# Kernel tuning notes

Hardware: AMD Instinct MI355X
Metric: run time of the kernel (lower is better)

Reference implementation:

```python
import jax, jax.numpy as jnp
import numpy as np

N_NODES = 100000
N_EDGES = 3200000
OUT_DIM = 128


def setup_inputs() -> dict:
    key = jax.random.key(0)
    k1, k2, k3, k4, k5, k6 = jax.random.split(key, 6)
    return {
        "previous_inclusion_score": jax.random.normal(k1, (N_NODES,), dtype=jnp.float32),
        "nodes": jax.random.normal(k2, (N_NODES, 3), dtype=jnp.float32),
        "row_indices": jax.random.randint(k3, (N_EDGES,), 0, N_NODES, dtype=jnp.int32),
        "col_indices": jax.random.randint(k4, (N_EDGES,), 0, N_NODES, dtype=jnp.int32),
        "W_phi": jax.random.normal(k5, (OUT_DIM,), dtype=jnp.float32),
        "W_theta": jax.random.normal(k6, (3, 1), dtype=jnp.float32),
    }


def reference(previous_inclusion_score, nodes, row_indices, col_indices, W_phi, W_theta):
    # gather endpoints and project 3D differences through W_theta: [E,3] @ [3,1] -> [E,1]
    diff = nodes[row_indices] - nodes[col_indices]
    proj = diff @ W_theta
    # torch.norm over dim=1 of an [E,1] tensor == abs
    neigh_distances = jnp.abs(proj[:, 0])  # [E]
    # per-node max over incident edges; empty segments -> -inf, original leaves them 0
    max_distances = jax.ops.segment_max(neigh_distances, row_indices, num_segments=N_NODES)
    max_distances = jnp.maximum(max_distances, 0.0)  # distances are >= 0, so this matches the zeros default
    # outer product with W_phi: [N, D]
    list_inc_score = W_phi[None, :] * max_distances[:, None]
    # previous_inclusion_score is non-empty and D != 1 -> mean over feature dim, then average with previous
    inc_mean = jnp.mean(list_inc_score, axis=1)  # [N]
    return 0.5 * (previous_inclusion_score + inc_mean)
```

## Files before the change

### kernel.cpp

```cpp
#include <hip/hip_runtime.h>

#define OUT_DIM 128
#define CHUNK_LG 14
#define CHUNK (1 << CHUNK_LG)
#define PB 64

typedef int          vint4  __attribute__((ext_vector_type(4)));
typedef unsigned int vuint4 __attribute__((ext_vector_type(4)));
typedef unsigned int u32;

__device__ __forceinline__ u32 enc15(float d) {
    u32 b = __float_as_uint(d);
    b += 0x7FFFu + ((b >> 16) & 1u);
    return (b >> 16) & 0x7FFFu;
}

__global__ void init_kernel(float* __restrict__ p, float* __restrict__ meanW,
                            const float* __restrict__ nodes,
                            const float* __restrict__ Wt,
                            const float* __restrict__ W_phi, int n) {
    int i = blockIdx.x * blockDim.x + threadIdx.x;
    if (i < n) {
        float x = nodes[3 * i], y = nodes[3 * i + 1], z = nodes[3 * i + 2];
        p[i] = x * Wt[0] + y * Wt[1] + z * Wt[2];
    }
    if (blockIdx.x == 0 && threadIdx.x == 0) {
        float s = 0.0f;
        #pragma unroll
        for (int j = 0; j < OUT_DIM; ++j) s += W_phi[j];
        *meanW = s / (float)OUT_DIM;
    }
}

__global__ void encode_kernel(const float* __restrict__ p,
                              const int* __restrict__ row,
                              const int* __restrict__ col,
                              u32* __restrict__ key, int E) {
    int t = blockIdx.x * blockDim.x + threadIdx.x;
    int base = t * 4;
    if (base >= E) return;
    if (base + 3 < E) {
        vint4 r = __builtin_nontemporal_load((const vint4*)(row + base));
        vint4 c = __builtin_nontemporal_load((const vint4*)(col + base));
        float d0 = fabsf(p[r.x] - p[c.x]);
        float d1 = fabsf(p[r.y] - p[c.y]);
        float d2 = fabsf(p[r.z] - p[c.z]);
        float d3 = fabsf(p[r.w] - p[c.w]);
        vuint4 k;
        k.x = ((u32)r.x << 15) | enc15(d0);
        k.y = ((u32)r.y << 15) | enc15(d1);
        k.z = ((u32)r.z << 15) | enc15(d2);
        k.w = ((u32)r.w << 15) | enc15(d3);
        *(vuint4*)(key + base) = k;
    } else {
        for (int e = base; e < E; ++e)
            key[e] = ((u32)row[e] << 15) | enc15(fabsf(p[row[e]] - p[col[e]]));
    }
}

#define PROC(V) do { \
        if ((V.x >> (15 + CHUNK_LG)) == upass) atomicMax(&lds[(V.x >> 15) & (CHUNK - 1)], V.x & 0x7FFFu); \
        if ((V.y >> (15 + CHUNK_LG)) == upass) atomicMax(&lds[(V.y >> 15) & (CHUNK - 1)], V.y & 0x7FFFu); \
        if ((V.z >> (15 + CHUNK_LG)) == upass) atomicMax(&lds[(V.z >> 15) & (CHUNK - 1)], V.z & 0x7FFFu); \
        if ((V.w >> (15 + CHUNK_LG)) == upass) atomicMax(&lds[(V.w >> 15) & (CHUNK - 1)], V.w & 0x7FFFu); \
    } while (0)

__global__ void chunkmax_kernel(const u32* __restrict__ key,
                                u32* __restrict__ partial, int E, int nch) {
    __shared__ u32 lds[CHUNK];
    int pass = blockIdx.x / PB;
    int b    = blockIdx.x % PB;
    for (int i = threadIdx.x; i < CHUNK; i += blockDim.x) lds[i] = 0;
    __syncthreads();

    int E4 = E >> 2;
    int per = (E4 + PB - 1) / PB;
    int s = b * per;
    int e = min(s + per, E4);
    const vuint4* key4 = (const vuint4*)key;
    u32 upass = (u32)pass;
    int step = (int)blockDim.x;
    int k = s + (int)threadIdx.x;
    for (; k + 3 * step < e; k += 4 * step) {
        vuint4 a0 = key4[k];
        vuint4 a1 = key4[k + step];
        vuint4 a2 = key4[k + 2 * step];
        vuint4 a3 = key4[k + 3 * step];
        PROC(a0); PROC(a1); PROC(a2); PROC(a3);
    }
    for (; k < e; k += step) {
        vuint4 a0 = key4[k];
        PROC(a0);
    }
    if (b == PB - 1) {
        for (int eidx = (E4 << 2) + (int)threadIdx.x; eidx < E; eidx += (int)blockDim.x) {
            u32 v = key[eidx];
            if ((v >> (15 + CHUNK_LG)) == upass) atomicMax(&lds[(v >> 15) & (CHUNK - 1)], v & 0x7FFFu);
        }
    }
    __syncthreads();
    u32* dst = partial + ((size_t)pass * PB + b) * (CHUNK / 2);
    for (int j = threadIdx.x; j < CHUNK / 2; j += blockDim.x)
        dst[j] = lds[2 * j] | (lds[2 * j + 1] << 16);
}

__global__ void reduce_final_kernel(const float* __restrict__ prev,
                                    const u32* __restrict__ partial,
                                    const float* __restrict__ meanW,
                                    float* __restrict__ out, int n) {
    int t = blockIdx.x * blockDim.x + threadIdx.x;
    int i0 = t * 2;
    if (i0 >= n) return;
    int chunk = i0 >> CHUNK_LG;
    int local = i0 & (CHUNK - 1);
    const u32* base = partial + (size_t)chunk * PB * (CHUNK / 2) + (local >> 1);
    u32 mlo = 0, mhi = 0;
    #pragma unroll
    for (int b = 0; b < PB; ++b) {
        u32 v = base[(size_t)b * (CHUNK / 2)];
        mlo = max(mlo, v & 0xFFFFu);
        mhi = max(mhi, v >> 16);
    }
    float mw = *meanW;
    float flo = __uint_as_float(mlo << 16);
    float fhi = __uint_as_float(mhi << 16);
    out[i0] = 0.5f * (prev[i0] + mw * flo);
    if (i0 + 1 < n)
        out[i0 + 1] = 0.5f * (prev[i0 + 1] + mw * fhi);
}

__global__ void fb_zero_kernel(float* __restrict__ maxd, float* __restrict__ p,
                               float* __restrict__ meanW,
                               const float* __restrict__ nodes,
                               const float* __restrict__ Wt,
                               const float* __restrict__ W_phi, int n) {
    int i = blockIdx.x * blockDim.x + threadIdx.x;
    if (i < n) {
        maxd[i] = 0.0f;
        float x = nodes[3 * i], y = nodes[3 * i + 1], z = nodes[3 * i + 2];
        p[i] = x * Wt[0] + y * Wt[1] + z * Wt[2];
    }
    if (blockIdx.x == 0 && threadIdx.x == 0) {
        float s = 0.0f;
        for (int j = 0; j < OUT_DIM; ++j) s += W_phi[j];
        *meanW = s / (float)OUT_DIM;
    }
}
__global__ void fb_edge_kernel(const float* __restrict__ p,
                               const int* __restrict__ row,
                               const int* __restrict__ col,
                               float* __restrict__ maxd, int E) {
    int t = blockIdx.x * blockDim.x + threadIdx.x;
    int base = t * 4;
    if (base >= E) return;
    if (base + 3 < E) {
        vint4 r = __builtin_nontemporal_load((const vint4*)(row + base));
        vint4 c = __builtin_nontemporal_load((const vint4*)(col + base));
        atomicMax((int*)&maxd[r.x], __float_as_int(fabsf(p[r.x] - p[c.x])));
        atomicMax((int*)&maxd[r.y], __float_as_int(fabsf(p[r.y] - p[c.y])));
        atomicMax((int*)&maxd[r.z], __float_as_int(fabsf(p[r.z] - p[c.z])));
        atomicMax((int*)&maxd[r.w], __float_as_int(fabsf(p[r.w] - p[c.w])));
    } else {
        for (int e = base; e < E; ++e) {
            float d = fabsf(p[row[e]] - p[col[e]]);
            atomicMax((int*)&maxd[row[e]], __float_as_int(d));
        }
    }
}
__global__ void fb_final_kernel(const float* __restrict__ prev,
                                const float* __restrict__ maxd,
                                const float* __restrict__ meanW,
                                float* __restrict__ out, int n) {
    int i = blockIdx.x * blockDim.x + threadIdx.x;
    if (i < n) out[i] = 0.5f * (prev[i] + (*meanW) * maxd[i]);
}

extern "C" void kernel_launch(void* const* d_in, const int* in_sizes, int n_in,
                              void* d_out, int out_size, void* d_ws, size_t ws_size,
                              hipStream_t stream) {
    const float* prev    = (const float*)d_in[0];
    const float* nodes   = (const float*)d_in[1];
    const int*   row     = (const int*)d_in[2];
    const int*   col     = (const int*)d_in[3];
    const float* W_phi   = (const float*)d_in[4];
    const float* W_theta = (const float*)d_in[5];

    const int N = in_sizes[0];
    const int E = in_sizes[2];
    float* out = (float*)d_out;
    const int B = 256;

    const int nch = (N + CHUNK - 1) >> CHUNK_LG;

    size_t pBytes    = ((size_t)N * 4 + 15) & ~(size_t)15;
    size_t keyBytes  = ((size_t)E * 4 + 15) & ~(size_t)15;
    size_t partBytes = (size_t)nch * PB * (CHUNK / 2) * 4;
    size_t need = pBytes + keyBytes + partBytes + 4;

    if (ws_size >= need) {
        float* p     = (float*)d_ws;
        u32*   key   = (u32*)((char*)d_ws + pBytes);
        u32*   part  = (u32*)((char*)d_ws + pBytes + keyBytes);
        float* meanW = (float*)((char*)d_ws + pBytes + keyBytes + partBytes);

        init_kernel<<<(N + B - 1) / B, B, 0, stream>>>(p, meanW, nodes, W_theta, W_phi, N);
        int tE = (E + 3) / 4;
        encode_kernel<<<(tE + B - 1) / B, B, 0, stream>>>(p, row, col, key, E);
        chunkmax_kernel<<<nch * PB, B, 0, stream>>>(key, part, E, nch);
        int tN = (N + 1) / 2;
        reduce_final_kernel<<<(tN + B - 1) / B, B, 0, stream>>>(prev, part, meanW, out, N);
    } else {
        float* p     = (float*)d_ws;
        float* maxd  = (float*)d_ws + N;
        float* meanW = (float*)d_ws + 2 * (size_t)N;
        fb_zero_kernel<<<(N + B - 1) / B, B, 0, stream>>>(maxd, p, meanW, nodes, W_theta, W_phi, N);
        int tE = (E + 3) / 4;
        fb_edge_kernel<<<(tE + B - 1) / B, B, 0, stream>>>(p, row, col, maxd, E);
        fb_final_kernel<<<(N + B - 1) / B, B, 0, stream>>>(prev, maxd, meanW, out, N);
    }
}
```

Before: 62.73 us.

## Bin edge keys by node chunk before LDS segment-max instead of rescanning all keys

The encode kernel becomes a binning kernel that builds keys in LDS, counts them per node chunk, reserves space through global atomic cursors and scatters each key into a per-chunk bucket. The chunk-max kernel then reads only its own chunk's bucket, so the key array is no longer read once per chunk (7 times for 100k nodes). PB drops from 64 to 48. The cost is a scattered write pattern, extra LDS passes, global atomics and a workspace of nch*E words. The fast path is also limited to N <= 2^17.

```diff
diff --git a/kernel.cpp b/kernel.cpp
--- a/kernel.cpp
+++ b/kernel.cpp
@@ -3,7 +3,9 @@
 #define OUT_DIM 128
 #define CHUNK_LG 14
 #define CHUNK (1 << CHUNK_LG)
-#define PB 64
+#define PB 48
+#define EPB 4096
+#define NCH_MAX 8
 
 typedef int          vint4  __attribute__((ext_vector_type(4)));
 typedef unsigned int vuint4 __attribute__((ext_vector_type(4)));
@@ -16,6 +18,7 @@
 }
 
 __global__ void init_kernel(float* __restrict__ p, float* __restrict__ meanW,
+                            u32* __restrict__ cursor,
                             const float* __restrict__ nodes,
                             const float* __restrict__ Wt,
                             const float* __restrict__ W_phi, int n) {
@@ -24,82 +27,115 @@
         float x = nodes[3 * i], y = nodes[3 * i + 1], z = nodes[3 * i + 2];
         p[i] = x * Wt[0] + y * Wt[1] + z * Wt[2];
     }
-    if (blockIdx.x == 0 && threadIdx.x == 0) {
-        float s = 0.0f;
-        #pragma unroll
-        for (int j = 0; j < OUT_DIM; ++j) s += W_phi[j];
-        *meanW = s / (float)OUT_DIM;
-    }
-}
-
-__global__ void encode_kernel(const float* __restrict__ p,
-                              const int* __restrict__ row,
-                              const int* __restrict__ col,
-                              u32* __restrict__ key, int E) {
-    int t = blockIdx.x * blockDim.x + threadIdx.x;
-    int base = t * 4;
-    if (base >= E) return;
-    if (base + 3 < E) {
-        vint4 r = __builtin_nontemporal_load((const vint4*)(row + base));
-        vint4 c = __builtin_nontemporal_load((const vint4*)(col + base));
-        float d0 = fabsf(p[r.x] - p[c.x]);
-        float d1 = fabsf(p[r.y] - p[c.y]);
-        float d2 = fabsf(p[r.z] - p[c.z]);
-        float d3 = fabsf(p[r.w] - p[c.w]);
-        vuint4 k;
-        k.x = ((u32)r.x << 15) | enc15(d0);
-        k.y = ((u32)r.y << 15) | enc15(d1);
-        k.z = ((u32)r.z << 15) | enc15(d2);
-        k.w = ((u32)r.w << 15) | enc15(d3);
-        *(vuint4*)(key + base) = k;
-    } else {
-        for (int e = base; e < E; ++e)
-            key[e] = ((u32)row[e] << 15) | enc15(fabsf(p[row[e]] - p[col[e]]));
-    }
-}
-
-#define PROC(V) do { \
-        if ((V.x >> (15 + CHUNK_LG)) == upass) atomicMax(&lds[(V.x >> 15) & (CHUNK - 1)], V.x & 0x7FFFu); \
-        if ((V.y >> (15 + CHUNK_LG)) == upass) atomicMax(&lds[(V.y >> 15) & (CHUNK - 1)], V.y & 0x7FFFu); \
-        if ((V.z >> (15 + CHUNK_LG)) == upass) atomicMax(&lds[(V.z >> 15) & (CHUNK - 1)], V.z & 0x7FFFu); \
-        if ((V.w >> (15 + CHUNK_LG)) == upass) atomicMax(&lds[(V.w >> 15) & (CHUNK - 1)], V.w & 0x7FFFu); \
-    } while (0)
-
-__global__ void chunkmax_kernel(const u32* __restrict__ key,
-                                u32* __restrict__ partial, int E, int nch) {
+    if (blockIdx.x == 0) {
+        if (threadIdx.x < NCH_MAX) cursor[threadIdx.x] = 0;
+        if (threadIdx.x == 0) {
+            float s = 0.0f;
+            #pragma unroll
+            for (int j = 0; j < OUT_DIM; ++j) s += W_phi[j];
+            *meanW = s / (float)OUT_DIM;
+        }
+    }
+}
+
+__global__ void bin_kernel(const float* __restrict__ p,
+                           const int* __restrict__ row,
+                           const int* __restrict__ col,
+                           u32* __restrict__ binned, u32* __restrict__ cursor,
+                           int E, int Epad) {
+    __shared__ u32 keys[EPB];
+    __shared__ u32 cnt[NCH_MAX];
+    __shared__ u32 base[NCH_MAX];
+    if (threadIdx.x < NCH_MAX) cnt[threadIdx.x] = 0;
+    __syncthreads();
+
+    int s = blockIdx.x * EPB;
+    int nk = min(EPB, E - s);
+
+    #pragma unroll
+    for (int r = 0; r < EPB / (256 * 4); ++r) {
+        int li  = r * 1024 + (int)threadIdx.x * 4;
+        int idx = s + li;
+        if (idx + 3 < E) {
+            vint4 rr = __builtin_nontemporal_load((const vint4*)(row + idx));
+            vint4 cc = __builtin_nontemporal_load((const vint4*)(col + idx));
+            keys[li + 0] = ((u32)rr.x << 15) | enc15(fabsf(p[rr.x] - p[cc.x]));
+            keys[li + 1] = ((u32)rr.y << 15) | enc15(fabsf(p[rr.y] - p[cc.y]));
+            keys[li + 2] = ((u32)rr.z << 15) | enc15(fabsf(p[rr.z] - p[cc.z]));
+            keys[li + 3] = ((u32)rr.w << 15) | enc15(fabsf(p[rr.w] - p[cc.w]));
+        } else {
+            for (int j = idx; j < E; ++j)
+                keys[j - s] = ((u32)row[j] << 15) | enc15(fabsf(p[row[j]] - p[col[j]]));
+        }
+    }
+    __syncthreads();
+
+    u32 lc[NCH_MAX] = {0, 0, 0, 0, 0, 0, 0, 0};
+    for (int i = threadIdx.x; i < nk; i += 256) lc[keys[i] >> (15 + CHUNK_LG)]++;
+    #pragma unroll
+    for (int c = 0; c < NCH_MAX; ++c)
+        if (lc[c]) atomicAdd(&cnt[c], lc[c]);
+    __syncthreads();
+
+    if (threadIdx.x < NCH_MAX) {
+        u32 t = cnt[threadIdx.x];
+        base[threadIdx.x] = t ? atomicAdd(&cursor[threadIdx.x], t) : 0;
+        cnt[threadIdx.x] = 0;
+    }
+    __syncthreads();
+
+    for (int i = threadIdx.x; i < nk; i += 256) {
+        u32 k = keys[i];
+        u32 c = k >> (15 + CHUNK_LG);
+        u32 o = atomicAdd(&cnt[c], 1u);
+        binned[(size_t)c * Epad + base[c] + o] = k;
+    }
+}
+
+__global__ void chunkmax_kernel(const u32* __restrict__ binned,
+                                const u32* __restrict__ cursor,
+                                u32* __restrict__ partial, int Epad) {
     __shared__ u32 lds[CHUNK];
-    int pass = blockIdx.x / PB;
-    int b    = blockIdx.x % PB;
+    int c = blockIdx.x / PB;
+    int b = blockIdx.x % PB;
     for (int i = threadIdx.x; i < CHUNK; i += blockDim.x) lds[i] = 0;
     __syncthreads();
 
-    int E4 = E >> 2;
-    int per = (E4 + PB - 1) / PB;
+    int cnt = (int)cursor[c];
+    const u32* bk = binned + (size_t)c * Epad;
+    int per = (((cnt + PB - 1) / PB) + 3) & ~3;
     int s = b * per;
-    int e = min(s + per, E4);
-    const vuint4* key4 = (const vuint4*)key;
-    u32 upass = (u32)pass;
+    int e = min(s + per, cnt);
+
+    int nv4 = (e - s) >> 2;
+    const vuint4* bk4 = (const vuint4*)(bk + s);
     int step = (int)blockDim.x;
-    int k = s + (int)threadIdx.x;
-    for (; k + 3 * step < e; k += 4 * step) {
-        vuint4 a0 = key4[k];
-        vuint4 a1 = key4[k + step];
-        vuint4 a2 = key4[k + 2 * step];
-        vuint4 a3 = key4[k + 3 * step];
-        PROC(a0); PROC(a1); PROC(a2); PROC(a3);
-    }
-    for (; k < e; k += step) {
-        vuint4 a0 = key4[k];
-        PROC(a0);
-    }
-    if (b == PB - 1) {
-        for (int eidx = (E4 << 2) + (int)threadIdx.x; eidx < E; eidx += (int)blockDim.x) {
-            u32 v = key[eidx];
-            if ((v >> (15 + CHUNK_LG)) == upass) atomicMax(&lds[(v >> 15) & (CHUNK - 1)], v & 0x7FFFu);
-        }
-    }
-    __syncthreads();
-    u32* dst = partial + ((size_t)pass * PB + b) * (CHUNK / 2);
+    int k = (int)threadIdx.x;
+    for (; k + step < nv4; k += 2 * step) {
+        vuint4 a0 = bk4[k];
+        vuint4 a1 = bk4[k + step];
+        atomicMax(&lds[(a0.x >> 15) & (CHUNK - 1)], a0.x & 0x7FFFu);
+        atomicMax(&lds[(a0.y >> 15) & (CHUNK - 1)], a0.y & 0x7FFFu);
+        atomicMax(&lds[(a0.z >> 15) & (CHUNK - 1)], a0.z & 0x7FFFu);
+        atomicMax(&lds[(a0.w >> 15) & (CHUNK - 1)], a0.w & 0x7FFFu);
+        atomicMax(&lds[(a1.x >> 15) & (CHUNK - 1)], a1.x & 0x7FFFu);
+        atomicMax(&lds[(a1.y >> 15) & (CHUNK - 1)], a1.y & 0x7FFFu);
+        atomicMax(&lds[(a1.z >> 15) & (CHUNK - 1)], a1.z & 0x7FFFu);
+        atomicMax(&lds[(a1.w >> 15) & (CHUNK - 1)], a1.w & 0x7FFFu);
+    }
+    for (; k < nv4; k += step) {
+        vuint4 a0 = bk4[k];
+        atomicMax(&lds[(a0.x >> 15) & (CHUNK - 1)], a0.x & 0x7FFFu);
+        atomicMax(&lds[(a0.y >> 15) & (CHUNK - 1)], a0.y & 0x7FFFu);
+        atomicMax(&lds[(a0.z >> 15) & (CHUNK - 1)], a0.z & 0x7FFFu);
+        atomicMax(&lds[(a0.w >> 15) & (CHUNK - 1)], a0.w & 0x7FFFu);
+    }
+    for (int j = s + (nv4 << 2) + (int)threadIdx.x; j < e; j += step) {
+        u32 v = bk[j];
+        atomicMax(&lds[(v >> 15) & (CHUNK - 1)], v & 0x7FFFu);
+    }
+    __syncthreads();
+    u32* dst = partial + ((size_t)c * PB + b) * (CHUNK / 2);
     for (int j = threadIdx.x; j < CHUNK / 2; j += blockDim.x)
         dst[j] = lds[2 * j] | (lds[2 * j + 1] << 16);
 }
@@ -190,23 +226,25 @@
     float* out = (float*)d_out;
     const int B = 256;
 
-    const int nch = (N + CHUNK - 1) >> CHUNK_LG;
+    const int nch  = (N + CHUNK - 1) >> CHUNK_LG;
+    const int Epad = (E + 3) & ~3;
 
     size_t pBytes    = ((size_t)N * 4 + 15) & ~(size_t)15;
-    size_t keyBytes  = ((size_t)E * 4 + 15) & ~(size_t)15;
+    size_t binBytes  = (size_t)nch * Epad * 4;
     size_t partBytes = (size_t)nch * PB * (CHUNK / 2) * 4;
-    size_t need = pBytes + keyBytes + partBytes + 4;
-
-    if (ws_size >= need) {
+    size_t need = pBytes + binBytes + partBytes + NCH_MAX * 4 + 4;
+
+    if (ws_size >= need && N <= (1 << 17) && nch <= NCH_MAX) {
         float* p     = (float*)d_ws;
-        u32*   key   = (u32*)((char*)d_ws + pBytes);
-        u32*   part  = (u32*)((char*)d_ws + pBytes + keyBytes);
-        float* meanW = (float*)((char*)d_ws + pBytes + keyBytes + partBytes);
-
-        init_kernel<<<(N + B - 1) / B, B, 0, stream>>>(p, meanW, nodes, W_theta, W_phi, N);
-        int tE = (E + 3) / 4;
-        encode_kernel<<<(tE + B - 1) / B, B, 0, stream>>>(p, row, col, key, E);
-        chunkmax_kernel<<<nch * PB, B, 0, stream>>>(key, part, E, nch);
+        u32*   binned= (u32*)((char*)d_ws + pBytes);
+        u32*   part  = (u32*)((char*)d_ws + pBytes + binBytes);
+        u32*   cursor= (u32*)((char*)d_ws + pBytes + binBytes + partBytes);
+        float* meanW = (float*)((char*)d_ws + pBytes + binBytes + partBytes + NCH_MAX * 4);
+
+        init_kernel<<<(N + B - 1) / B, B, 0, stream>>>(p, meanW, cursor, nodes, W_theta, W_phi, N);
+        int nbB = (E + EPB - 1) / EPB;
+        bin_kernel<<<nbB, B, 0, stream>>>(p, row, col, binned, cursor, E, Epad);
+        chunkmax_kernel<<<nch * PB, B, 0, stream>>>(binned, cursor, part, Epad);
         int tN = (N + 1) / 2;
         reduce_final_kernel<<<(tN + B - 1) / B, B, 0, stream>>>(prev, part, meanW, out, N);
     } else {
```

Result: slower. 77.31 us (+23.2%).

## Bin edge keys per chunk with wave ballots so chunkmax reads only its bin

Applied to the files above, without the earlier changes.

Replaces the encode pass with a binning kernel in which each wave computes keys and compacts them into per-chunk regions using ballot and popcount prefix offsets. The chunkmax kernel then reads only the keys belonging to its chunk, instead of every block scanning all keys and filtering them for each pass. This cuts the chunkmax read traffic by about a factor of the chunk count. In exchange it adds scattered per-wave writes, a serial loop over chunks per round, non-vectorized loads, a workspace sized NWAVES*nch*EW, and a change of PB from 64 to 48.

```diff
diff --git a/kernel.cpp b/kernel.cpp
--- a/kernel.cpp
+++ b/kernel.cpp
@@ -3,11 +3,13 @@
 #define OUT_DIM 128
 #define CHUNK_LG 14
 #define CHUNK (1 << CHUNK_LG)
-#define PB 64
+#define PB 48
+#define NWAVES 4096
+#define NCH_MAX 8
 
 typedef int          vint4  __attribute__((ext_vector_type(4)));
-typedef unsigned int vuint4 __attribute__((ext_vector_type(4)));
 typedef unsigned int u32;
+typedef unsigned long long u64;
 
 __device__ __forceinline__ u32 enc15(float d) {
     u32 b = __float_as_uint(d);
@@ -32,74 +34,75 @@
     }
 }
 
-__global__ void encode_kernel(const float* __restrict__ p,
-                              const int* __restrict__ row,
-                              const int* __restrict__ col,
-                              u32* __restrict__ key, int E) {
-    int t = blockIdx.x * blockDim.x + threadIdx.x;
-    int base = t * 4;
-    if (base >= E) return;
-    if (base + 3 < E) {
-        vint4 r = __builtin_nontemporal_load((const vint4*)(row + base));
-        vint4 c = __builtin_nontemporal_load((const vint4*)(col + base));
-        float d0 = fabsf(p[r.x] - p[c.x]);
-        float d1 = fabsf(p[r.y] - p[c.y]);
-        float d2 = fabsf(p[r.z] - p[c.z]);
-        float d3 = fabsf(p[r.w] - p[c.w]);
-        vuint4 k;
-        k.x = ((u32)r.x << 15) | enc15(d0);
-        k.y = ((u32)r.y << 15) | enc15(d1);
-        k.z = ((u32)r.z << 15) | enc15(d2);
-        k.w = ((u32)r.w << 15) | enc15(d3);
-        *(vuint4*)(key + base) = k;
-    } else {
-        for (int e = base; e < E; ++e)
-            key[e] = ((u32)row[e] << 15) | enc15(fabsf(p[row[e]] - p[col[e]]));
-    }
-}
-
-#define PROC(V) do { \
-        if ((V.x >> (15 + CHUNK_LG)) == upass) atomicMax(&lds[(V.x >> 15) & (CHUNK - 1)], V.x & 0x7FFFu); \
-        if ((V.y >> (15 + CHUNK_LG)) == upass) atomicMax(&lds[(V.y >> 15) & (CHUNK - 1)], V.y & 0x7FFFu); \
-        if ((V.z >> (15 + CHUNK_LG)) == upass) atomicMax(&lds[(V.z >> 15) & (CHUNK - 1)], V.z & 0x7FFFu); \
-        if ((V.w >> (15 + CHUNK_LG)) == upass) atomicMax(&lds[(V.w >> 15) & (CHUNK - 1)], V.w & 0x7FFFu); \
-    } while (0)
-
-__global__ void chunkmax_kernel(const u32* __restrict__ key,
-                                u32* __restrict__ partial, int E, int nch) {
+template<int NCH>
+__global__ void bin_kernel(const float* __restrict__ p,
+                           const int* __restrict__ row,
+                           const int* __restrict__ col,
+                           u32* __restrict__ reg, u32* __restrict__ cnt,
+                           int E, int EW, int rounds) {
+    int wid  = (int)((blockIdx.x * blockDim.x + threadIdx.x) >> 6);
+    int lane = (int)(threadIdx.x & 63);
+    long base = (long)wid * EW;
+    u32* myreg = reg + (size_t)wid * NCH * EW;
+
+    u32 cur[NCH];
+    #pragma unroll
+    for (int c = 0; c < NCH; ++c) cur[c] = 0;
+
+    u64 ltmask = ((u64)1 << lane) - 1;
+
+    for (int r = 0; r < rounds; ++r) {
+        long idx = base + (long)r * 64 + lane;
+        u32 key = 0;
+        int cl = -1;
+        if (idx < E) {
+            int rr = __builtin_nontemporal_load(row + idx);
+            int cc = __builtin_nontemporal_load(col + idx);
+            key = ((u32)rr << 15) | enc15(fabsf(p[rr] - p[cc]));
+            cl = rr >> CHUNK_LG;
+        }
+        #pragma unroll
+        for (int c = 0; c < NCH; ++c) {
+            u64 m = __ballot(cl == c);
+            if (m) {
+                if (cl == c) {
+                    int off = (int)__popcll(m & ltmask);
+                    myreg[(size_t)c * EW + cur[c] + off] = key;
+                }
+                cur[c] += (u32)__popcll(m);
+            }
+        }
+    }
+    if (lane == 0) {
+        #pragma unroll
+        for (int c = 0; c < NCH; ++c) cnt[(size_t)wid * NCH + c] = cur[c];
+    }
+}
+
+template<int NCH>
+__global__ void chunkmax_kernel(const u32* __restrict__ reg,
+                                const u32* __restrict__ cnt,
+                                u32* __restrict__ partial, int EW, int per) {
     __shared__ u32 lds[CHUNK];
-    int pass = blockIdx.x / PB;
-    int b    = blockIdx.x % PB;
+    int c = blockIdx.x / PB;
+    int b = blockIdx.x % PB;
     for (int i = threadIdx.x; i < CHUNK; i += blockDim.x) lds[i] = 0;
     __syncthreads();
 
-    int E4 = E >> 2;
-    int per = (E4 + PB - 1) / PB;
-    int s = b * per;
-    int e = min(s + per, E4);
-    const vuint4* key4 = (const vuint4*)key;
-    u32 upass = (u32)pass;
-    int step = (int)blockDim.x;
-    int k = s + (int)threadIdx.x;
-    for (; k + 3 * step < e; k += 4 * step) {
-        vuint4 a0 = key4[k];
-        vuint4 a1 = key4[k + step];
-        vuint4 a2 = key4[k + 2 * step];
-        vuint4 a3 = key4[k + 3 * step];
-        PROC(a0); PROC(a1); PROC(a2); PROC(a3);
-    }
-    for (; k < e; k += step) {
-        vuint4 a0 = key4[k];
-        PROC(a0);
-    }
-    if (b == PB - 1) {
-        for (int eidx = (E4 << 2) + (int)threadIdx.x; eidx < E; eidx += (int)blockDim.x) {
-            u32 v = key[eidx];
-            if ((v >> (15 + CHUNK_LG)) == upass) atomicMax(&lds[(v >> 15) & (CHUNK - 1)], v & 0x7FFFu);
+    int wave = (int)(threadIdx.x >> 6);
+    int lane = (int)(threadIdx.x & 63);
+    int w0 = b * per;
+    int w1 = min(w0 + per, NWAVES);
+    for (int w = w0 + wave; w < w1; w += 4) {
+        int n = (int)cnt[(size_t)w * NCH + c];
+        const u32* r = reg + ((size_t)w * NCH + c) * EW;
+        for (int j = lane; j < n; j += 64) {
+            u32 v = r[j];
+            atomicMax(&lds[(v >> 15) & (CHUNK - 1)], v & 0x7FFFu);
         }
     }
     __syncthreads();
-    u32* dst = partial + ((size_t)pass * PB + b) * (CHUNK / 2);
+    u32* dst = partial + ((size_t)c * PB + b) * (CHUNK / 2);
     for (int j = threadIdx.x; j < CHUNK / 2; j += blockDim.x)
         dst[j] = lds[2 * j] | (lds[2 * j + 1] << 16);
 }
@@ -191,22 +194,38 @@
     const int B = 256;
 
     const int nch = (N + CHUNK - 1) >> CHUNK_LG;
+    int EW = ((E + NWAVES - 1) / NWAVES + 63) & ~63;
+    if (EW == 0) EW = 64;
+    const int rounds = EW / 64;
+    const int per = (NWAVES + PB - 1) / PB;
 
     size_t pBytes    = ((size_t)N * 4 + 15) & ~(size_t)15;
-    size_t keyBytes  = ((size_t)E * 4 + 15) & ~(size_t)15;
+    size_t regBytes  = (size_t)NWAVES * nch * EW * 4;
+    size_t cntBytes  = ((size_t)NWAVES * nch * 4 + 15) & ~(size_t)15;
     size_t partBytes = (size_t)nch * PB * (CHUNK / 2) * 4;
-    size_t need = pBytes + keyBytes + partBytes + 4;
-
-    if (ws_size >= need) {
-        float* p     = (float*)d_ws;
-        u32*   key   = (u32*)((char*)d_ws + pBytes);
-        u32*   part  = (u32*)((char*)d_ws + pBytes + keyBytes);
-        float* meanW = (float*)((char*)d_ws + pBytes + keyBytes + partBytes);
+    size_t need = pBytes + regBytes + cntBytes + partBytes + 4;
+
+    if (ws_size >= need && nch >= 1 && nch <= NCH_MAX) {
+        float* p    = (float*)d_ws;
+        u32*   reg  = (u32*)((char*)d_ws + pBytes);
+        u32*   cnt  = (u32*)((char*)d_ws + pBytes + regBytes);
+        u32*   part = (u32*)((char*)d_ws + pBytes + regBytes + cntBytes);
+        float* meanW= (float*)((char*)d_ws + pBytes + regBytes + cntBytes + partBytes);
 
         init_kernel<<<(N + B - 1) / B, B, 0, stream>>>(p, meanW, nodes, W_theta, W_phi, N);
-        int tE = (E + 3) / 4;
-        encode_kernel<<<(tE + B - 1) / B, B, 0, stream>>>(p, row, col, key, E);
-        chunkmax_kernel<<<nch * PB, B, 0, stream>>>(key, part, E, nch);
+
+        int binBlocks = NWAVES * 64 / B;
+        switch (nch) {
+        #define LAUNCH_CASE(NC) \
+            case NC: \
+                bin_kernel<NC><<<binBlocks, B, 0, stream>>>(p, row, col, reg, cnt, E, EW, rounds); \
+                chunkmax_kernel<NC><<<NC * PB, B, 0, stream>>>(reg, cnt, part, EW, per); \
+                break;
+            LAUNCH_CASE(1) LAUNCH_CASE(2) LAUNCH_CASE(3) LAUNCH_CASE(4)
+            LAUNCH_CASE(5) LAUNCH_CASE(6) LAUNCH_CASE(7) LAUNCH_CASE(8)
+        #undef LAUNCH_CASE
+        }
+
         int tN = (N + 1) / 2;
         reduce_final_kernel<<<(tN + B - 1) / B, B, 0, stream>>>(prev, part, meanW, out, N);
     } else {
```

Result: slower. 84.15 us (+34.1%).
